# Performance work log

Measured on AMD Instinct MI355X. Metric: run time of the kernel, lower is better.

Reference implementation:

```python
import jax, jax.numpy as jnp
import numpy as np

D_MODEL = 1024
NUM_HEADS = 16
D_K = D_MODEL // NUM_HEADS  # 64
B, S = 4, 1024


def setup_inputs() -> dict:
    key = jax.random.key(0)
    ks = jax.random.split(key, 8)
    scale = 1.0 / np.sqrt(D_MODEL)
    return {
        "query": jax.random.normal(ks[0], (B, S, D_MODEL), dtype=jnp.float32),
        "key": jax.random.normal(ks[1], (B, S, D_MODEL), dtype=jnp.float32),
        "value": jax.random.normal(ks[2], (B, S, D_MODEL), dtype=jnp.float32),
        "mask": jnp.ones((B, S, S), dtype=jnp.int32),
        # per-head projection weights, stacked: [H, d_model, d_k]
        "Wq": jax.random.normal(ks[3], (NUM_HEADS, D_MODEL, D_K), dtype=jnp.float32) * scale,
        "Wk": jax.random.normal(ks[4], (NUM_HEADS, D_MODEL, D_K), dtype=jnp.float32) * scale,
        "Wv": jax.random.normal(ks[5], (NUM_HEADS, D_MODEL, D_K), dtype=jnp.float32) * scale,
        # out projection: [H*d_v, d_model]
        "Wo": jax.random.normal(ks[6], (NUM_HEADS * D_K, D_MODEL), dtype=jnp.float32) * scale,
    }


def reference(query, key, value, mask, Wq, Wk, Wv, Wo):
    H, _, d_k = Wq.shape
    b, s, _ = query.shape
    inv_sqrt_dk = 1.0 / np.sqrt(d_k).astype(np.float32)
    # per-head projections (vectorized over heads): [H, B, S, d_k]
    q = jnp.einsum("bsd,hdk->hbsk", query, Wq)
    k = jnp.einsum("bsd,hdk->hbsk", key, Wk)
    v = jnp.einsum("bsd,hdk->hbsk", value, Wv)
    # raw scores before masking are what the torch module returns as q_key_dots
    scores = jnp.einsum("hbqk,hbmk->hbqm", q, k) * inv_sqrt_dk  # [H,B,Sq,Sk]
    masked = jnp.where(mask[None, :, :, :] == 0, -jnp.inf, scores)
    p_attn = jax.nn.softmax(masked, axis=-1)
    attn_out = jnp.einsum("hbqm,hbmk->hbqk", p_attn, v)  # [H,B,S,d_k]
    # concat heads along last dim in head order (matches torch.cat over h)
    concat = jnp.transpose(attn_out, (1, 2, 0, 3)).reshape(b, s, H * d_k)
    out = concat @ Wo  # [B,S,d_model]
    # torch returns (out, list of per-head masked scores); stack as [H,B,S,S]
    return out, masked
```

## Files before the change

kernel.cpp:

```cpp
#include <hip/hip_runtime.h>
#include <hip/hip_bf16.h>
#include <math.h>

typedef __attribute__((ext_vector_type(8))) short short8;
typedef __attribute__((ext_vector_type(4))) float f32x4;


static __device__ __forceinline__ unsigned short f2bf(float x) {
  union { float f; unsigned u; } v; v.f = x;
  unsigned r = v.u + 0x7fffu + ((v.u >> 16) & 1u);
  return (unsigned short)(r >> 16);
}

static __device__ __forceinline__ void bar_lds() {
  asm volatile("s_waitcnt lgkmcnt(0)" ::: "memory");
  __builtin_amdgcn_s_barrier();
}

__global__ __launch_bounds__(256) void prep_wt(
    const float* __restrict__ Wq, const float* __restrict__ Wk,
    const float* __restrict__ Wv, const float* __restrict__ Wo,
    unsigned short* __restrict__ wt, unsigned short* __restrict__ wot) {
  if (blockIdx.x < 3072) {
    int idx = blockIdx.x * 256 + threadIdx.x;
    int which = idx >> 18;
    int rem = idx & 262143;
    int h = rem >> 14;
    int d = (rem >> 4) & 1023;
    int n4 = rem & 15;
    const float* W = which == 0 ? Wq : (which == 1 ? Wk : Wv);
    float4 v = *(const float4*)(W + (size_t)h * 65536 + (size_t)d * 64 + n4 * 4);
    unsigned short* dst = wt + (size_t)which * 1048576 + ((size_t)h * 64 + n4 * 4) * 1024 + d;
    dst[0]    = f2bf(v.x);
    dst[1024] = f2bf(v.y);
    dst[2048] = f2bf(v.z);
    dst[3072] = f2bf(v.w);
  } else {
    int idx = (blockIdx.x - 3072) * 256 + threadIdx.x;
    int k = idx >> 8;
    int n4 = idx & 255;
    float4 v = *(const float4*)(Wo + (size_t)k * 1024 + n4 * 4);
    unsigned short* dst = wot + ((size_t)n4 * 4) * 1024 + k;
    dst[0]    = f2bf(v.x);
    dst[1024] = f2bf(v.y);
    dst[2048] = f2bf(v.z);
    dst[3072] = f2bf(v.w);
  }
}

__global__ __launch_bounds__(256) void proj_kernel(
    const float* __restrict__ q_in, const float* __restrict__ k_in,
    const float* __restrict__ v_in, const unsigned short* __restrict__ wt,
    unsigned short* __restrict__ qws, unsigned short* __restrict__ kws,
    unsigned short* __restrict__ vws) {
  __shared__ unsigned short lds[(64 + 256) * 72];
  unsigned short* Xs = lds;
  unsigned short* Ws = lds + 64 * 72;
  const int tid = threadIdx.x;
  const int s0 = blockIdx.x * 64;
  const int hg = blockIdx.y;
  const int b = blockIdx.z & 3;
  const int which = blockIdx.z >> 2;
  const float* X = which == 0 ? q_in : (which == 1 ? k_in : v_in);
  const unsigned short* wbase = wt + (size_t)which * 1048576 + (size_t)hg * 256 * 1024;
  const int w = tid >> 6, lane = tid & 63, q16 = lane & 15, quad = lane >> 4;

  f32x4 acc[4][4];
  #pragma unroll
  for (int m = 0; m < 4; ++m)
    #pragma unroll
    for (int j = 0; j < 4; ++j) acc[m][j] = (f32x4)0.0f;

  for (int kt = 0; kt < 16; ++kt) {
    #pragma unroll
    for (int p = 0; p < 4; ++p) {
      int idx = tid + p * 256;
      int r = idx >> 4, c4 = idx & 15;
      const float4 v = *(const float4*)(X + (size_t)(b * 1024 + s0 + r) * 1024 + kt * 64 + c4 * 4);
      ushort4 u;
      u.x = f2bf(v.x); u.y = f2bf(v.y); u.z = f2bf(v.z); u.w = f2bf(v.w);
      *(ushort4*)&Xs[r * 72 + c4 * 4] = u;
    }
    #pragma unroll
    for (int p = 0; p < 8; ++p) {
      int idx = tid + p * 256;
      int r = idx >> 3, c = idx & 7;
      *(uint4*)&Ws[r * 72 + c * 8] = *(const uint4*)(wbase + (size_t)r * 1024 + kt * 64 + c * 8);
    }
    __syncthreads();
    #pragma unroll
    for (int kk = 0; kk < 2; ++kk) {
      short8 a[4];
      #pragma unroll
      for (int m = 0; m < 4; ++m)
        a[m] = *(const short8*)&Xs[(m * 16 + q16) * 72 + kk * 32 + quad * 8];
      #pragma unroll
      for (int j = 0; j < 4; ++j) {
        short8 bb = *(const short8*)&Ws[(w * 64 + j * 16 + q16) * 72 + kk * 32 + quad * 8];
        #pragma unroll
        for (int m = 0; m < 4; ++m)
          acc[m][j] = __builtin_amdgcn_mfma_f32_16x16x32_bf16(a[m], bb, acc[m][j], 0, 0, 0);
      }
    }
    __syncthreads();
  }

  if (which != 2) {
    unsigned short* Cs = lds;
    #pragma unroll
    for (int m = 0; m < 4; ++m)
      #pragma unroll
      for (int j = 0; j < 4; ++j)
        #pragma unroll
        for (int r = 0; r < 4; ++r)
          Cs[(m * 16 + quad * 4 + r) * 264 + w * 64 + j * 16 + q16] = f2bf(acc[m][j][r]);
    __syncthreads();
    unsigned short* dst = which ? kws : qws;
    #pragma unroll
    for (int p = 0; p < 8; ++p) {
      int idx = tid + p * 256;
      int sl = idx >> 5, t = idx & 31;
      int nl = t * 8;
      int head = hg * 4 + (nl >> 6), ko = nl & 63;
      *(uint4*)(dst + ((size_t)((b * 16 + head) * 1024 + s0 + sl)) * 64 + ko) =
          *(const uint4*)&Cs[sl * 264 + nl];
    }
  } else {
    unsigned short* Cs = lds;
    #pragma unroll
    for (int m = 0; m < 4; ++m)
      #pragma unroll
      for (int j = 0; j < 4; ++j)
        #pragma unroll
        for (int r = 0; r < 4; ++r)
          Cs[(w * 64 + j * 16 + q16) * 72 + m * 16 + quad * 4 + r] = f2bf(acc[m][j][r]);
    __syncthreads();
    #pragma unroll
    for (int p = 0; p < 8; ++p) {
      int idx = tid + p * 256;
      int nl = idx >> 3, c = idx & 7;
      int head = hg * 4 + (nl >> 6), d = nl & 63;
      *(uint4*)(vws + ((size_t)((b * 16 + head) * 64 + d)) * 1024 + s0 + c * 8) =
          *(const uint4*)&Cs[nl * 72 + c * 8];
    }
  }
}

__global__ __launch_bounds__(256) void attn_kernel(
    const unsigned short* __restrict__ qws, const unsigned short* __restrict__ kws,
    const unsigned short* __restrict__ vws, const int* __restrict__ mask,
    float* __restrict__ scores, unsigned short* __restrict__ cws) {
  __shared__ unsigned short Qs[64 * 72];
  __shared__ unsigned short Ks[64 * 72];
  __shared__ unsigned short Vts[64 * 72];
  __shared__ unsigned short Ps[64 * 72];
  const int tid = threadIdx.x;
  const int L = blockIdx.x;
  const int xcd = L & 7, t = L >> 3;
  const int h = (((t >> 3) & 3) << 2) | (xcd & 3);
  const int qt = ((t & 7) << 1) | (xcd >> 2);
  const int b = t >> 5;
  const int q0 = qt * 64;
  const int w = tid >> 6, lane = tid & 63, q16 = lane & 15, quad = lane >> 4;
  const size_t bh = (size_t)(b * 16 + h);

  const int r1 = tid >> 3, c1 = tid & 7;
  const int r2 = (tid + 256) >> 3;
  const unsigned short* ksrc0 = kws + bh * 1024 * 64;
  const unsigned short* vsrc0 = vws + bh * 64 * 1024;

  {
    const unsigned short* src = qws + (bh * 1024 + q0) * 64;
    *(uint4*)&Qs[r1 * 72 + c1 * 8] = *(const uint4*)(src + r1 * 64 + c1 * 8);
    *(uint4*)&Qs[r2 * 72 + c1 * 8] = *(const uint4*)(src + r2 * 64 + c1 * 8);
  }
  uint4 kr0 = *(const uint4*)(ksrc0 + r1 * 64 + c1 * 8);
  uint4 kr1 = *(const uint4*)(ksrc0 + r2 * 64 + c1 * 8);
  uint4 vr0 = *(const uint4*)(vsrc0 + (size_t)r1 * 1024 + c1 * 8);
  uint4 vr1 = *(const uint4*)(vsrc0 + (size_t)r2 * 1024 + c1 * 8);

  bar_lds();
  short8 aq0 = *(const short8*)&Qs[(w * 16 + q16) * 72 + quad * 8];
  short8 aq1 = *(const short8*)&Qs[(w * 16 + q16) * 72 + 32 + quad * 8];

  f32x4 o[4];
  #pragma unroll
  for (int j = 0; j < 4; ++j) o[j] = (f32x4)0.0f;
  float m_run[4] = {-3.0e38f, -3.0e38f, -3.0e38f, -3.0e38f};
  float l_run[4] = {0.f, 0.f, 0.f, 0.f};

  for (int kt = 0; kt < 16; ++kt) {
    *(uint4*)&Ks[r1 * 72 + c1 * 8] = kr0;
    *(uint4*)&Ks[r2 * 72 + c1 * 8] = kr1;
    *(uint4*)&Vts[r1 * 72 + c1 * 8] = vr0;
    *(uint4*)&Vts[r2 * 72 + c1 * 8] = vr1;
    if (kt < 15) {
      const unsigned short* ksrc = ksrc0 + (size_t)(kt + 1) * 64 * 64;
      const unsigned short* vsrc = vsrc0 + (kt + 1) * 64;
      kr0 = *(const uint4*)(ksrc + r1 * 64 + c1 * 8);
      kr1 = *(const uint4*)(ksrc + r2 * 64 + c1 * 8);
      vr0 = *(const uint4*)(vsrc + (size_t)r1 * 1024 + c1 * 8);
      vr1 = *(const uint4*)(vsrc + (size_t)r2 * 1024 + c1 * 8);
    }
    bar_lds();

    f32x4 sacc[4];
    #pragma unroll
    for (int j = 0; j < 4; ++j) sacc[j] = (f32x4)0.0f;
    #pragma unroll
    for (int j = 0; j < 4; ++j) {
      short8 bb = *(const short8*)&Ks[(j * 16 + q16) * 72 + quad * 8];
      sacc[j] = __builtin_amdgcn_mfma_f32_16x16x32_bf16(aq0, bb, sacc[j], 0, 0, 0);
    }
    #pragma unroll
    for (int j = 0; j < 4; ++j) {
      short8 bb = *(const short8*)&Ks[(j * 16 + q16) * 72 + 32 + quad * 8];
      sacc[j] = __builtin_amdgcn_mfma_f32_16x16x32_bf16(aq1, bb, sacc[j], 0, 0, 0);
    }

    float rm[4] = {-3.0e38f, -3.0e38f, -3.0e38f, -3.0e38f};
    #pragma unroll
    for (int j = 0; j < 4; ++j) {
      #pragma unroll
      for (int r = 0; r < 4; ++r) {
        int ql = w * 16 + quad * 4 + r;
        int q = q0 + ql;
        int key = kt * 64 + j * 16 + q16;
        int mk = mask[((size_t)b * 1024 + q) * 1024 + key];
        float sv = sacc[j][r] * 0.125f;
        scores[(((size_t)h * 4 + b) * 1024 + q) * 1024 + key] = mk ? sv : -INFINITY;
        sv = mk ? sv : -3.0e38f;
        sacc[j][r] = sv;
        rm[r] = fmaxf(rm[r], sv);
      }
    }
    #pragma unroll
    for (int mM = 1; mM <= 8; mM <<= 1) {
      #pragma unroll
      for (int r = 0; r < 4; ++r) rm[r] = fmaxf(rm[r], __shfl_xor(rm[r], mM));
    }
    int need = 0;
    #pragma unroll
    for (int r = 0; r < 4; ++r) need |= (rm[r] > m_run[r] + 8.0f);
    if (__any(need)) {
      #pragma unroll
      for (int r = 0; r < 4; ++r) {
        float mnew = fmaxf(m_run[r], rm[r]);
        float alpha = __expf(m_run[r] - mnew);
        m_run[r] = mnew;
        l_run[r] *= alpha;
        #pragma unroll
        for (int j = 0; j < 4; ++j) o[j][r] *= alpha;
      }
    }
    float rs[4] = {0.f, 0.f, 0.f, 0.f};
    #pragma unroll
    for (int j = 0; j < 4; ++j) {
      #pragma unroll
      for (int r = 0; r < 4; ++r) {
        float p = __expf(sacc[j][r] - m_run[r]);
        rs[r] += p;
        int ql = w * 16 + quad * 4 + r;
        Ps[ql * 72 + j * 16 + q16] = f2bf(p);
      }
    }
    #pragma unroll
    for (int mM = 1; mM <= 8; mM <<= 1) {
      #pragma unroll
      for (int r = 0; r < 4; ++r) rs[r] += __shfl_xor(rs[r], mM);
    }
    #pragma unroll
    for (int r = 0; r < 4; ++r) l_run[r] += rs[r];

    #pragma unroll
    for (int kk = 0; kk < 2; ++kk) {
      short8 a = *(const short8*)&Ps[(w * 16 + q16) * 72 + kk * 32 + quad * 8];
      #pragma unroll
      for (int j = 0; j < 4; ++j) {
        short8 bb = *(const short8*)&Vts[(j * 16 + q16) * 72 + kk * 32 + quad * 8];
        o[j] = __builtin_amdgcn_mfma_f32_16x16x32_bf16(a, bb, o[j], 0, 0, 0);
      }
    }
    bar_lds();
  }

  float inv[4];
  #pragma unroll
  for (int r = 0; r < 4; ++r) inv[r] = 1.0f / l_run[r];
  #pragma unroll
  for (int j = 0; j < 4; ++j) {
    #pragma unroll
    for (int r = 0; r < 4; ++r) {
      int ql = w * 16 + quad * 4 + r;
      int d = j * 16 + q16;
      cws[((size_t)(b * 1024 + q0 + ql)) * 1024 + h * 64 + d] = f2bf(o[j][r] * inv[r]);
    }
  }
}

__global__ __launch_bounds__(256) void outproj_kernel(
    const unsigned short* __restrict__ cws, const unsigned short* __restrict__ wot,
    float* __restrict__ out) {
  __shared__ unsigned short As[64 * 72];
  __shared__ unsigned short Bs[64 * 72];
  const int tid = threadIdx.x;
  const int m0 = blockIdx.x * 64;
  const int n0 = blockIdx.y * 64;
  const int w = tid >> 6, lane = tid & 63, q16 = lane & 15, quad = lane >> 4;
  f32x4 acc[4];
  #pragma unroll
  for (int j = 0; j < 4; ++j) acc[j] = (f32x4)0.0f;

  for (int kt = 0; kt < 16; ++kt) {
    #pragma unroll
    for (int p = 0; p < 2; ++p) {
      int idx = tid + p * 256, r = idx >> 3, c = idx & 7;
      *(uint4*)&As[r * 72 + c * 8] = *(const uint4*)(cws + (size_t)(m0 + r) * 1024 + kt * 64 + c * 8);
      *(uint4*)&Bs[r * 72 + c * 8] = *(const uint4*)(wot + (size_t)(n0 + r) * 1024 + kt * 64 + c * 8);
    }
    __syncthreads();
    #pragma unroll
    for (int kk = 0; kk < 2; ++kk) {
      short8 a = *(const short8*)&As[(w * 16 + q16) * 72 + kk * 32 + quad * 8];
      #pragma unroll
      for (int j = 0; j < 4; ++j) {
        short8 bb = *(const short8*)&Bs[(j * 16 + q16) * 72 + kk * 32 + quad * 8];
        acc[j] = __builtin_amdgcn_mfma_f32_16x16x32_bf16(a, bb, acc[j], 0, 0, 0);
      }
    }
    __syncthreads();
  }
  #pragma unroll
  for (int j = 0; j < 4; ++j) {
    #pragma unroll
    for (int r = 0; r < 4; ++r) {
      out[(size_t)(m0 + w * 16 + quad * 4 + r) * 1024 + n0 + j * 16 + q16] = acc[j][r];
    }
  }
}

extern "C" void kernel_launch(void* const* d_in, const int* in_sizes, int n_in,
                              void* d_out, int out_size, void* d_ws, size_t ws_size,
                              hipStream_t stream) {
  (void)in_sizes; (void)n_in; (void)out_size; (void)ws_size;
  const float* q_in = (const float*)d_in[0];
  const float* k_in = (const float*)d_in[1];
  const float* v_in = (const float*)d_in[2];
  const int* mask   = (const int*)d_in[3];
  const float* Wq   = (const float*)d_in[4];
  const float* Wk   = (const float*)d_in[5];
  const float* Wv   = (const float*)d_in[6];
  const float* Wo   = (const float*)d_in[7];

  float* out = (float*)d_out;
  float* scores = out + (size_t)4 * 1024 * 1024;

  unsigned short* qws = (unsigned short*)d_ws;
  unsigned short* kws = qws + (size_t)4 * 16 * 1024 * 64;
  unsigned short* vws = kws + (size_t)4 * 16 * 1024 * 64;
  unsigned short* cws = vws + (size_t)4 * 16 * 1024 * 64;
  unsigned short* wt  = cws;
  unsigned short* wot = cws + (size_t)4 * 1024 * 1024;

  prep_wt<<<dim3(4096), 256, 0, stream>>>(Wq, Wk, Wv, Wo, wt, wot);
  proj_kernel<<<dim3(16, 4, 12), 256, 0, stream>>>(q_in, k_in, v_in, wt, qws, kws, vws);
  attn_kernel<<<dim3(1024), 256, 0, stream>>>(qws, kws, vws, mask, scores, cws);
  outproj_kernel<<<dim3(64, 16), 256, 0, stream>>>(cws, wot, out);
}
```

Before: 519.4 us.

## Register-prefetch tiles in projections, stage mask in LDS, enlarge outproj tiles

The projection and output-projection GEMMs now prefetch the next K-tile into registers while the current one is computed, so global loads overlap MFMA work. The attention kernel loads mask tiles with coalesced int4 reads into LDS instead of scattered per-element global reads, and writes the scores with nontemporal stores. The output projection moves to 128x128 tiles with 512 threads. Together these aim to cut memory latency stalls, at the cost of more registers and LDS that may lower occupancy.

```diff
diff --git a/kernel.cpp b/kernel.cpp
--- a/kernel.cpp
+++ b/kernel.cpp
@@ -71,23 +71,45 @@
     #pragma unroll
     for (int j = 0; j < 4; ++j) acc[m][j] = (f32x4)0.0f;
 
+  float4 xr[4];
+  uint4 wreg[8];
+  #pragma unroll
+  for (int p = 0; p < 4; ++p) {
+    int idx = tid + p * 256, r = idx >> 4, c4 = idx & 15;
+    xr[p] = *(const float4*)(X + (size_t)(b * 1024 + s0 + r) * 1024 + c4 * 4);
+  }
+  #pragma unroll
+  for (int p = 0; p < 8; ++p) {
+    int idx = tid + p * 256, r = idx >> 3, c = idx & 7;
+    wreg[p] = *(const uint4*)(wbase + (size_t)r * 1024 + c * 8);
+  }
+
   for (int kt = 0; kt < 16; ++kt) {
     #pragma unroll
     for (int p = 0; p < 4; ++p) {
-      int idx = tid + p * 256;
-      int r = idx >> 4, c4 = idx & 15;
-      const float4 v = *(const float4*)(X + (size_t)(b * 1024 + s0 + r) * 1024 + kt * 64 + c4 * 4);
+      int idx = tid + p * 256, r = idx >> 4, c4 = idx & 15;
       ushort4 u;
-      u.x = f2bf(v.x); u.y = f2bf(v.y); u.z = f2bf(v.z); u.w = f2bf(v.w);
+      u.x = f2bf(xr[p].x); u.y = f2bf(xr[p].y); u.z = f2bf(xr[p].z); u.w = f2bf(xr[p].w);
       *(ushort4*)&Xs[r * 72 + c4 * 4] = u;
     }
     #pragma unroll
     for (int p = 0; p < 8; ++p) {
-      int idx = tid + p * 256;
-      int r = idx >> 3, c = idx & 7;
-      *(uint4*)&Ws[r * 72 + c * 8] = *(const uint4*)(wbase + (size_t)r * 1024 + kt * 64 + c * 8);
-    }
-    __syncthreads();
+      int idx = tid + p * 256, r = idx >> 3, c = idx & 7;
+      *(uint4*)&Ws[r * 72 + c * 8] = wreg[p];
+    }
+    if (kt < 15) {
+      #pragma unroll
+      for (int p = 0; p < 4; ++p) {
+        int idx = tid + p * 256, r = idx >> 4, c4 = idx & 15;
+        xr[p] = *(const float4*)(X + (size_t)(b * 1024 + s0 + r) * 1024 + (kt + 1) * 64 + c4 * 4);
+      }
+      #pragma unroll
+      for (int p = 0; p < 8; ++p) {
+        int idx = tid + p * 256, r = idx >> 3, c = idx & 7;
+        wreg[p] = *(const uint4*)(wbase + (size_t)r * 1024 + (kt + 1) * 64 + c * 8);
+      }
+    }
+    bar_lds();
     #pragma unroll
     for (int kk = 0; kk < 2; ++kk) {
       short8 a[4];
@@ -102,7 +124,7 @@
           acc[m][j] = __builtin_amdgcn_mfma_f32_16x16x32_bf16(a[m], bb, acc[m][j], 0, 0, 0);
       }
     }
-    __syncthreads();
+    bar_lds();
   }
 
   if (which != 2) {
@@ -154,6 +176,7 @@
   __shared__ unsigned short Ks[64 * 72];
   __shared__ unsigned short Vts[64 * 72];
   __shared__ unsigned short Ps[64 * 72];
+  __shared__ int Ms[64 * 68];
   const int tid = threadIdx.x;
   const int L = blockIdx.x;
   const int xcd = L & 7, t = L >> 3;
@@ -168,6 +191,7 @@
   const int r2 = (tid + 256) >> 3;
   const unsigned short* ksrc0 = kws + bh * 1024 * 64;
   const unsigned short* vsrc0 = vws + bh * 64 * 1024;
+  const int* msrc0 = mask + ((size_t)b * 1024 + q0) * 1024;
 
   {
     const unsigned short* src = qws + (bh * 1024 + q0) * 64;
@@ -178,6 +202,12 @@
   uint4 kr1 = *(const uint4*)(ksrc0 + r2 * 64 + c1 * 8);
   uint4 vr0 = *(const uint4*)(vsrc0 + (size_t)r1 * 1024 + c1 * 8);
   uint4 vr1 = *(const uint4*)(vsrc0 + (size_t)r2 * 1024 + c1 * 8);
+  int4 mr[4];
+  #pragma unroll
+  for (int p = 0; p < 4; ++p) {
+    int idx = tid + p * 256, r = idx >> 4, c4 = idx & 15;
+    mr[p] = *(const int4*)(msrc0 + (size_t)r * 1024 + c4 * 4);
+  }
 
   bar_lds();
   short8 aq0 = *(const short8*)&Qs[(w * 16 + q16) * 72 + quad * 8];
@@ -194,6 +224,11 @@
     *(uint4*)&Ks[r2 * 72 + c1 * 8] = kr1;
     *(uint4*)&Vts[r1 * 72 + c1 * 8] = vr0;
     *(uint4*)&Vts[r2 * 72 + c1 * 8] = vr1;
+    #pragma unroll
+    for (int p = 0; p < 4; ++p) {
+      int idx = tid + p * 256, r = idx >> 4, c4 = idx & 15;
+      *(int4*)&Ms[r * 68 + c4 * 4] = mr[p];
+    }
     if (kt < 15) {
       const unsigned short* ksrc = ksrc0 + (size_t)(kt + 1) * 64 * 64;
       const unsigned short* vsrc = vsrc0 + (kt + 1) * 64;
@@ -201,6 +236,11 @@
       kr1 = *(const uint4*)(ksrc + r2 * 64 + c1 * 8);
       vr0 = *(const uint4*)(vsrc + (size_t)r1 * 1024 + c1 * 8);
       vr1 = *(const uint4*)(vsrc + (size_t)r2 * 1024 + c1 * 8);
+      #pragma unroll
+      for (int p = 0; p < 4; ++p) {
+        int idx = tid + p * 256, r = idx >> 4, c4 = idx & 15;
+        mr[p] = *(const int4*)(msrc0 + (size_t)r * 1024 + (kt + 1) * 64 + c4 * 4);
+      }
     }
     bar_lds();
 
@@ -226,9 +266,10 @@
         int ql = w * 16 + quad * 4 + r;
         int q = q0 + ql;
         int key = kt * 64 + j * 16 + q16;
-        int mk = mask[((size_t)b * 1024 + q) * 1024 + key];
+        int mk = Ms[ql * 68 + j * 16 + q16];
         float sv = sacc[j][r] * 0.125f;
-        scores[(((size_t)h * 4 + b) * 1024 + q) * 1024 + key] = mk ? sv : -INFINITY;
+        __builtin_nontemporal_store(mk ? sv : -INFINITY,
+            &scores[(((size_t)h * 4 + b) * 1024 + q) * 1024 + key]);
         sv = mk ? sv : -3.0e38f;
         sacc[j][r] = sv;
         rm[r] = fmaxf(rm[r], sv);
@@ -298,43 +339,72 @@
   }
 }
 
-__global__ __launch_bounds__(256) void outproj_kernel(
+__global__ __launch_bounds__(512) void outproj_kernel(
     const unsigned short* __restrict__ cws, const unsigned short* __restrict__ wot,
     float* __restrict__ out) {
-  __shared__ unsigned short As[64 * 72];
-  __shared__ unsigned short Bs[64 * 72];
+  __shared__ unsigned short As[128 * 72];
+  __shared__ unsigned short Bs[128 * 72];
   const int tid = threadIdx.x;
-  const int m0 = blockIdx.x * 64;
-  const int n0 = blockIdx.y * 64;
+  const int m0 = blockIdx.x * 128;
+  const int n0 = blockIdx.y * 128;
   const int w = tid >> 6, lane = tid & 63, q16 = lane & 15, quad = lane >> 4;
-  f32x4 acc[4];
-  #pragma unroll
-  for (int j = 0; j < 4; ++j) acc[j] = (f32x4)0.0f;
+  const int wr = w >> 2, wc = w & 3;
+  f32x4 acc[4][2];
+  #pragma unroll
+  for (int m = 0; m < 4; ++m)
+    #pragma unroll
+    for (int j = 0; j < 2; ++j) acc[m][j] = (f32x4)0.0f;
+
+  uint4 ar[2], br[2];
+  #pragma unroll
+  for (int p = 0; p < 2; ++p) {
+    int idx = tid + p * 512, r = idx >> 3, c = idx & 7;
+    ar[p] = *(const uint4*)(cws + (size_t)(m0 + r) * 1024 + c * 8);
+    br[p] = *(const uint4*)(wot + (size_t)(n0 + r) * 1024 + c * 8);
+  }
 
   for (int kt = 0; kt < 16; ++kt) {
     #pragma unroll
     for (int p = 0; p < 2; ++p) {
-      int idx = tid + p * 256, r = idx >> 3, c = idx & 7;
-      *(uint4*)&As[r * 72 + c * 8] = *(const uint4*)(cws + (size_t)(m0 + r) * 1024 + kt * 64 + c * 8);
-      *(uint4*)&Bs[r * 72 + c * 8] = *(const uint4*)(wot + (size_t)(n0 + r) * 1024 + kt * 64 + c * 8);
-    }
-    __syncthreads();
+      int idx = tid + p * 512, r = idx >> 3, c = idx & 7;
+      *(uint4*)&As[r * 72 + c * 8] = ar[p];
+      *(uint4*)&Bs[r * 72 + c * 8] = br[p];
+    }
+    if (kt < 15) {
+      #pragma unroll
+      for (int p = 0; p < 2; ++p) {
+        int idx = tid + p * 512, r = idx >> 3, c = idx & 7;
+        ar[p] = *(const uint4*)(cws + (size_t)(m0 + r) * 1024 + (kt + 1) * 64 + c * 8);
+        br[p] = *(const uint4*)(wot + (size_t)(n0 + r) * 1024 + (kt + 1) * 64 + c * 8);
+      }
+    }
+    bar_lds();
     #pragma unroll
     for (int kk = 0; kk < 2; ++kk) {
-      short8 a = *(const short8*)&As[(w * 16 + q16) * 72 + kk * 32 + quad * 8];
-      #pragma unroll
-      for (int j = 0; j < 4; ++j) {
-        short8 bb = *(const short8*)&Bs[(j * 16 + q16) * 72 + kk * 32 + quad * 8];
-        acc[j] = __builtin_amdgcn_mfma_f32_16x16x32_bf16(a, bb, acc[j], 0, 0, 0);
-      }
-    }
-    __syncthreads();
-  }
-  #pragma unroll
-  for (int j = 0; j < 4; ++j) {
-    #pragma unroll
-    for (int r = 0; r < 4; ++r) {
-      out[(size_t)(m0 + w * 16 + quad * 4 + r) * 1024 + n0 + j * 16 + q16] = acc[j][r];
+      short8 a[4];
+      #pragma unroll
+      for (int m = 0; m < 4; ++m)
+        a[m] = *(const short8*)&As[(wr * 64 + m * 16 + q16) * 72 + kk * 32 + quad * 8];
+      #pragma unroll
+      for (int j = 0; j < 2; ++j) {
+        short8 bb = *(const short8*)&Bs[(wc * 32 + j * 16 + q16) * 72 + kk * 32 + quad * 8];
+        #pragma unroll
+        for (int m = 0; m < 4; ++m)
+          acc[m][j] = __builtin_amdgcn_mfma_f32_16x16x32_bf16(a[m], bb, acc[m][j], 0, 0, 0);
+      }
+    }
+    bar_lds();
+  }
+  #pragma unroll
+  for (int m = 0; m < 4; ++m) {
+    #pragma unroll
+    for (int j = 0; j < 2; ++j) {
+      #pragma unroll
+      for (int r = 0; r < 4; ++r) {
+        __builtin_nontemporal_store(acc[m][j][r],
+            &out[(size_t)(m0 + wr * 64 + m * 16 + quad * 4 + r) * 1024 +
+                 n0 + wc * 32 + j * 16 + q16]);
+      }
     }
   }
 }
@@ -365,5 +435,5 @@
   prep_wt<<<dim3(4096), 256, 0, stream>>>(Wq, Wk, Wv, Wo, wt, wot);
   proj_kernel<<<dim3(16, 4, 12), 256, 0, stream>>>(q_in, k_in, v_in, wt, qws, kws, vws);
   attn_kernel<<<dim3(1024), 256, 0, stream>>>(qws, kws, vws, mask, scores, cws);
-  outproj_kernel<<<dim3(64, 16), 256, 0, stream>>>(cws, wot, out);
-}
+  outproj_kernel<<<dim3(32, 8), 512, 0, stream>>>(cws, wot, out);
+}
```

Measured after the change: 727.2 us. 40.0% more time.
